# Kernel optimization log

Hardware: AMD Instinct MI355X
Metric: run time of the kernel (lower is better)

The kernel has to match this reference:

```python
import jax, jax.numpy as jnp
import numpy as np


def setup_inputs() -> dict:
    key = jax.random.key(0)
    k1, k2, k3, k4 = jax.random.split(key, 4)
    B, H, S, E, L = 2, 12, 256, 64, 25
    return {
        "attention_probs": jax.random.uniform(k1, (B, H, S, S), dtype=jnp.float32),
        "value_attentions": jax.random.normal(k2, (B, H, S, E), dtype=jnp.float32),
        "relative_positions": jax.random.normal(k3, (B, S, S, H * E), dtype=jnp.float32),
        "W": jax.random.normal(k4, (L, H * E), dtype=jnp.float32) * 0.02,
        "b": jnp.zeros((L,), dtype=jnp.float32),
    }


def reference(attention_probs, value_attentions, relative_positions, W, b):
    # Faithful translation of TransformerMHSLayer.forward:
    #   out[b,h,i,j,e] = p[b,h,i,j] * (v[b,h,j,e] + rel[b,i,j,h,e])
    #   pre[b,j,i,l]   = sum_{h,e} out[b,h,i,j,e] * W[l, h*E+e] + bias[l]
    #   logits[b,j,l,i] = pre[b,j,i,l]
    B, H, S, E = value_attentions.shape
    L = W.shape[0]
    Wr = W.reshape(L, H, E)                       # [L,H,E], matches h*E+e flattening
    rel = relative_positions.reshape(B, S, S, H, E)  # view(B,S,S,H,E)
    # value term: contract v with W per head, then weight by attention probs
    pre = jnp.einsum('bhij,bhje,lhe->bjil', attention_probs, value_attentions, Wr)
    # relative-position term (same attention weighting)
    pre = pre + jnp.einsum('bhij,bijhe,lhe->bjil', attention_probs, rel, Wr)
    pre = pre + b                                  # bias over label dim
    return pre.transpose(0, 1, 3, 2)               # [B, S(j), L, S(i)]
```

## Files before the change

kernel.cpp:

```cpp
#include <hip/hip_runtime.h>
#include <stdint.h>


#define Bb 2
#define Hh 12
#define Ss 256
#define Ee 64
#define Ll 25
#define Kk 768

typedef __attribute__((ext_vector_type(8))) short bf16x8;
typedef __attribute__((ext_vector_type(4))) float f32x4;

#define NFRAG (Hh * 4)
#define AB_BYTES ((size_t)NFRAG * 64 * 8 * 2)
#define PT_BYTES ((size_t)Bb * Ss * Hh * Ss * 4)
#define WV_BYTES ((size_t)Bb * Ss * Hh * 32 * 4)

__device__ __forceinline__ ushort f2bf(float x) {
    union { float f; uint32_t u; } u; u.f = x;
    uint32_t r = u.u + 0x7fff + ((u.u >> 16) & 1);
    return (ushort)(r >> 16);
}

__global__ void a_pack_kernel(const float* __restrict__ W, ushort* __restrict__ ab) {
    int idx = blockIdx.x * 256 + threadIdx.x;
    if (idx >= NFRAG * 64) return;
    int lane = idx & 63, fi = idx >> 6;
    int Lt = fi & 1, ks = (fi >> 1) & 1, h = fi >> 2;
    int l = Lt * 16 + (lane & 15);
    int k0 = h * Ee + ks * 32 + (lane >> 4) * 8;
    ushort* dst = ab + (size_t)idx * 8;
#pragma unroll
    for (int t = 0; t < 8; ++t)
        dst[t] = (l < Ll) ? f2bf(W[l * Kk + k0 + t]) : (ushort)0;
}

__global__ void p_transpose_kernel(const float* __restrict__ p,
                                   float* __restrict__ pt) {
    __shared__ float tile[32][33];
    const int bh = blockIdx.y;
    const int b = bh / Hh, h = bh % Hh;
    const int ti = blockIdx.x >> 3, tj = blockIdx.x & 7;
    const int tx = threadIdx.x & 31, ty = threadIdx.x >> 5;
#pragma unroll
    for (int s = 0; s < 4; ++s) {
        const int il = ty + 8 * s;
        tile[il][tx] = p[((size_t)(b * Hh + h) * Ss + ti * 32 + il) * Ss + tj * 32 + tx];
    }
    __syncthreads();
#pragma unroll
    for (int s = 0; s < 4; ++s) {
        const int jl = ty + 8 * s;
        pt[((size_t)(b * Ss + tj * 32 + jl) * Hh + h) * Ss + ti * 32 + tx] = tile[tx][jl];
    }
}

__global__ void wv_kernel(const float* __restrict__ W, const float* __restrict__ v,
                          float* __restrict__ wv) {
    const int bj = blockIdx.x;
    const int b = bj >> 8, j = bj & (Ss - 1);
    const int t = threadIdx.x;
    const int h = t >> 5, l = t & 31;
    float acc = 0.f;
    if (l < Ll) {
        const float* wrow = W + l * Kk + h * Ee;
        const float* vrow = v + ((size_t)(b * Hh + h) * Ss + j) * Ee;
#pragma unroll
        for (int e = 0; e < Ee; ++e) acc = __builtin_fmaf(wrow[e], vrow[e], acc);
    }
    wv[((size_t)bj * Hh + h) * 32 + l] = acc;
}

struct Ops {
    float4 c0, c1, c2, c3;
    bf16x8 A00, A01, A10, A11;
    float4 w0, w1;
    float pv;
};

__global__ __launch_bounds__(256, 4) void mhs_pipe(
    const float* __restrict__ pt,
    const float* __restrict__ rel,
    const ushort* __restrict__ ab,
    const float* __restrict__ wv,
    const float* __restrict__ bias,
    float* __restrict__ out)
{
    const int g = blockIdx.x;
    const int ig = g & 3, j = (g >> 2) & (Ss - 1), b = g >> 10;
    const int tid = threadIdx.x;
    const int w = tid >> 6, lane = tid & 63;
    const int col = lane & 15, grp = lane >> 4;
    const int iw = ig * 64 + w * 16 + col;

    const float* relp = rel + ((size_t)(b * Ss + iw) * Ss + j) * Kk + grp * 8;
    const ushort* abl = ab + lane * 8;
    const float* wvb = wv + ((size_t)(b * Ss + j) * Hh) * 32 + grp * 4;
    const float* ptb = pt + ((size_t)(b * Ss + j) * Hh) * Ss + iw;

    f32x4 acc0 = {0.f, 0.f, 0.f, 0.f};
    f32x4 acc1 = {0.f, 0.f, 0.f, 0.f};

    auto load_ops = [&](Ops& o, int h) {
        const float* rb = relp + h * Ee;
        o.c0 = *(const float4*)(rb);
        o.c1 = *(const float4*)(rb + 4);
        o.c2 = *(const float4*)(rb + 32);
        o.c3 = *(const float4*)(rb + 36);
        const ushort* ap = abl + (size_t)h * 2048;
        o.A00 = *(const bf16x8*)(ap);
        o.A01 = *(const bf16x8*)(ap + 512);
        o.A10 = *(const bf16x8*)(ap + 1024);
        o.A11 = *(const bf16x8*)(ap + 1536);
        const float* wp = wvb + h * 32;
        o.w0 = *(const float4*)(wp);
        o.w1 = *(const float4*)(wp + 16);
        o.pv = ptb[h * Ss];
    };

    auto compute = [&](const Ops& o) {
        bf16x8 B0, B1;
#pragma unroll
        for (int t = 0; t < 4; ++t) {
            B0[t]     = (short)f2bf(((const float*)&o.c0)[t]);
            B0[t + 4] = (short)f2bf(((const float*)&o.c1)[t]);
            B1[t]     = (short)f2bf(((const float*)&o.c2)[t]);
            B1[t + 4] = (short)f2bf(((const float*)&o.c3)[t]);
        }
        f32x4 C0 = {0.f, 0.f, 0.f, 0.f}, C1 = {0.f, 0.f, 0.f, 0.f};
        C0 = __builtin_amdgcn_mfma_f32_16x16x32_bf16(o.A00, B0, C0, 0, 0, 0);
        C0 = __builtin_amdgcn_mfma_f32_16x16x32_bf16(o.A10, B1, C0, 0, 0, 0);
        C1 = __builtin_amdgcn_mfma_f32_16x16x32_bf16(o.A01, B0, C1, 0, 0, 0);
        C1 = __builtin_amdgcn_mfma_f32_16x16x32_bf16(o.A11, B1, C1, 0, 0, 0);
        const f32x4 wv0 = {o.w0.x, o.w0.y, o.w0.z, o.w0.w};
        const f32x4 wv1 = {o.w1.x, o.w1.y, o.w1.z, o.w1.w};
        acc0 += o.pv * (C0 + wv0);
        acc1 += o.pv * (C1 + wv1);
    };

    Ops oa, ob;
    load_ops(oa, 0);
#pragma unroll 1
    for (int h = 0; h < Hh; h += 2) {
        load_ops(ob, h + 1);
        compute(oa);
        load_ops(oa, (h + 2 < Hh) ? h + 2 : Hh - 1);
        compute(ob);
    }

#pragma unroll
    for (int r = 0; r < 4; ++r) {
        const int l0 = grp * 4 + r;
        out[((size_t)(b * Ss + j) * Ll + l0) * Ss + iw] = acc0[r] + bias[l0];
        const int l1 = 16 + grp * 4 + r;
        if (l1 < Ll)
            out[((size_t)(b * Ss + j) * Ll + l1) * Ss + iw] = acc1[r] + bias[l1];
    }
}

__global__ __launch_bounds__(256, 4) void mhs_basic(
    const float* __restrict__ p, const float* __restrict__ v,
    const float* __restrict__ rel, const float* __restrict__ W,
    const float* __restrict__ bias, float* __restrict__ out)
{
    const int g = blockIdx.x;
    const int ig = g & 3, j = (g >> 2) & (Ss - 1), b = g >> 10;
    const int tid = threadIdx.x;
    const int w = tid >> 6, lane = tid & 63;
    const int col = lane & 15, grp = lane >> 4;
    const int iw = ig * 64 + w * 16 + col;
    const float* relp = rel + ((size_t)(b * Ss + iw) * Ss + j) * Kk + grp * 8;

    f32x4 acc0 = {0.f, 0.f, 0.f, 0.f}, acc1 = {0.f, 0.f, 0.f, 0.f};
#pragma unroll 1
    for (int h = 0; h < Hh; ++h) {
        bf16x8 A00, A01, A10, A11;
#pragma unroll
        for (int t = 0; t < 8; ++t) {
            const int kb = h * Ee + grp * 8 + t;
            const int la = col, lb = 16 + col;
            A00[t] = (short)f2bf(W[la * Kk + kb]);
            A01[t] = (lb < Ll) ? (short)f2bf(W[lb * Kk + kb]) : (short)0;
            A10[t] = (short)f2bf(W[la * Kk + kb + 32]);
            A11[t] = (lb < Ll) ? (short)f2bf(W[lb * Kk + kb + 32]) : (short)0;
        }
        const float* vbp = v + ((size_t)(b * Hh + h) * Ss + j) * Ee + grp * 8;
        const float4 va0 = *(const float4*)(vbp);
        const float4 va1 = *(const float4*)(vbp + 4);
        const float4 vc0 = *(const float4*)(vbp + 32);
        const float4 vc1 = *(const float4*)(vbp + 36);
        const float* rb = relp + h * Ee;
        const float4 c0 = *(const float4*)(rb);
        const float4 c1 = *(const float4*)(rb + 4);
        const float4 c2 = *(const float4*)(rb + 32);
        const float4 c3 = *(const float4*)(rb + 36);
        const float pv = p[((size_t)(b * Hh + h) * Ss + iw) * Ss + j];
        bf16x8 B0, B1;
#pragma unroll
        for (int t = 0; t < 4; ++t) {
            B0[t]     = (short)f2bf(((const float*)&c0)[t] + ((const float*)&va0)[t]);
            B0[t + 4] = (short)f2bf(((const float*)&c1)[t] + ((const float*)&va1)[t]);
            B1[t]     = (short)f2bf(((const float*)&c2)[t] + ((const float*)&vc0)[t]);
            B1[t + 4] = (short)f2bf(((const float*)&c3)[t] + ((const float*)&vc1)[t]);
        }
        f32x4 C0 = {0.f, 0.f, 0.f, 0.f}, C1 = {0.f, 0.f, 0.f, 0.f};
        C0 = __builtin_amdgcn_mfma_f32_16x16x32_bf16(A00, B0, C0, 0, 0, 0);
        C0 = __builtin_amdgcn_mfma_f32_16x16x32_bf16(A10, B1, C0, 0, 0, 0);
        C1 = __builtin_amdgcn_mfma_f32_16x16x32_bf16(A01, B0, C1, 0, 0, 0);
        C1 = __builtin_amdgcn_mfma_f32_16x16x32_bf16(A11, B1, C1, 0, 0, 0);
        acc0 += pv * C0;
        acc1 += pv * C1;
    }
#pragma unroll
    for (int r = 0; r < 4; ++r) {
        const int l0 = grp * 4 + r;
        out[((size_t)(b * Ss + j) * Ll + l0) * Ss + iw] = acc0[r] + bias[l0];
        const int l1 = 16 + grp * 4 + r;
        if (l1 < Ll)
            out[((size_t)(b * Ss + j) * Ll + l1) * Ss + iw] = acc1[r] + bias[l1];
    }
}

extern "C" void kernel_launch(void* const* d_in, const int* in_sizes, int n_in,
                              void* d_out, int out_size, void* d_ws, size_t ws_size,
                              hipStream_t stream) {
    const float* p    = (const float*)d_in[0];
    const float* v    = (const float*)d_in[1];
    const float* rel  = (const float*)d_in[2];
    const float* W    = (const float*)d_in[3];
    const float* bias = (const float*)d_in[4];
    float* out = (float*)d_out;

    const int nblk = Bb * Ss * 4;
    const bool full = ws_size >= AB_BYTES + PT_BYTES + WV_BYTES;

    if (full) {
        ushort* ab = (ushort*)d_ws;
        float* pt = (float*)((char*)d_ws + AB_BYTES);
        float* wvp = (float*)((char*)d_ws + AB_BYTES + PT_BYTES);
        hipLaunchKernelGGL(a_pack_kernel, dim3((NFRAG * 64 + 255) / 256), dim3(256),
                           0, stream, W, ab);
        hipLaunchKernelGGL(p_transpose_kernel, dim3(64, Bb * Hh), dim3(256),
                           0, stream, p, pt);
        hipLaunchKernelGGL(wv_kernel, dim3(Bb * Ss), dim3(Hh * 32),
                           0, stream, W, v, wvp);
        hipLaunchKernelGGL(mhs_pipe, dim3(nblk), dim3(256), 0, stream,
                           pt, rel, ab, wvp, bias, out);
    } else {
        hipLaunchKernelGGL(mhs_basic, dim3(nblk), dim3(256), 0, stream,
                           p, v, rel, W, bias, out);
    }
}
```

Baseline: 124.5 us.

## Fold attention prob into B operand, accumulate in MFMA, swizzle block order

Scales the rel values by the attention prob before bf16 conversion so the MFMAs accumulate straight into acc0/acc1. This removes the per-head zeroed temporaries and the vector multiply-add after each head. The value term (p·wv) moves out of the pipelined loop into a separate post-loop reduction, which shrinks the per-head register buffer. Block indices are also remapped in an interleaved order to change which j/b tiles run concurrently, likely for cache or memory-channel locality. Rounding the p-scaled product to bf16 changes numerics slightly, and the post-loop reads p and wv a second time.

```diff
diff --git a/kernel.cpp b/kernel.cpp
--- a/kernel.cpp
+++ b/kernel.cpp
@@ -72,14 +72,13 @@
     wv[((size_t)bj * Hh + h) * 32 + l] = acc;
 }
 
-struct Ops {
-    float4 c0, c1, c2, c3;
+struct Buf {
+    float4 r0, r1, r2, r3;
     bf16x8 A00, A01, A10, A11;
-    float4 w0, w1;
     float pv;
 };
 
-__global__ __launch_bounds__(256, 4) void mhs_pipe(
+__global__ __launch_bounds__(256, 4) void mhs_pipe2(
     const float* __restrict__ pt,
     const float* __restrict__ rel,
     const ushort* __restrict__ ab,
@@ -87,8 +86,8 @@
     const float* __restrict__ bias,
     float* __restrict__ out)
 {
-    const int g = blockIdx.x;
-    const int ig = g & 3, j = (g >> 2) & (Ss - 1), b = g >> 10;
+    const int m = (blockIdx.x & 7) * 256 + (blockIdx.x >> 3);
+    const int ig = m & 3, j = (m >> 2) & (Ss - 1), b = m >> 10;
     const int tid = threadIdx.x;
     const int w = tid >> 6, lane = tid & 63;
     const int col = lane & 15, grp = lane >> 4;
@@ -96,58 +95,64 @@
 
     const float* relp = rel + ((size_t)(b * Ss + iw) * Ss + j) * Kk + grp * 8;
     const ushort* abl = ab + lane * 8;
+    const float* ptb = pt + ((size_t)(b * Ss + j) * Hh) * Ss + iw;
     const float* wvb = wv + ((size_t)(b * Ss + j) * Hh) * 32 + grp * 4;
-    const float* ptb = pt + ((size_t)(b * Ss + j) * Hh) * Ss + iw;
 
     f32x4 acc0 = {0.f, 0.f, 0.f, 0.f};
     f32x4 acc1 = {0.f, 0.f, 0.f, 0.f};
 
-    auto load_ops = [&](Ops& o, int h) {
+    auto load = [&](Buf& o, int h) {
         const float* rb = relp + h * Ee;
-        o.c0 = *(const float4*)(rb);
-        o.c1 = *(const float4*)(rb + 4);
-        o.c2 = *(const float4*)(rb + 32);
-        o.c3 = *(const float4*)(rb + 36);
+        o.r0 = *(const float4*)(rb);
+        o.r1 = *(const float4*)(rb + 4);
+        o.r2 = *(const float4*)(rb + 32);
+        o.r3 = *(const float4*)(rb + 36);
         const ushort* ap = abl + (size_t)h * 2048;
         o.A00 = *(const bf16x8*)(ap);
         o.A01 = *(const bf16x8*)(ap + 512);
         o.A10 = *(const bf16x8*)(ap + 1024);
         o.A11 = *(const bf16x8*)(ap + 1536);
-        const float* wp = wvb + h * 32;
-        o.w0 = *(const float4*)(wp);
-        o.w1 = *(const float4*)(wp + 16);
         o.pv = ptb[h * Ss];
     };
 
-    auto compute = [&](const Ops& o) {
+    auto compute = [&](const Buf& o) {
+        const float s = o.pv;
         bf16x8 B0, B1;
 #pragma unroll
         for (int t = 0; t < 4; ++t) {
-            B0[t]     = (short)f2bf(((const float*)&o.c0)[t]);
-            B0[t + 4] = (short)f2bf(((const float*)&o.c1)[t]);
-            B1[t]     = (short)f2bf(((const float*)&o.c2)[t]);
-            B1[t + 4] = (short)f2bf(((const float*)&o.c3)[t]);
+            B0[t]     = (short)f2bf(s * ((const float*)&o.r0)[t]);
+            B0[t + 4] = (short)f2bf(s * ((const float*)&o.r1)[t]);
+            B1[t]     = (short)f2bf(s * ((const float*)&o.r2)[t]);
+            B1[t + 4] = (short)f2bf(s * ((const float*)&o.r3)[t]);
         }
-        f32x4 C0 = {0.f, 0.f, 0.f, 0.f}, C1 = {0.f, 0.f, 0.f, 0.f};
-        C0 = __builtin_amdgcn_mfma_f32_16x16x32_bf16(o.A00, B0, C0, 0, 0, 0);
-        C0 = __builtin_amdgcn_mfma_f32_16x16x32_bf16(o.A10, B1, C0, 0, 0, 0);
-        C1 = __builtin_amdgcn_mfma_f32_16x16x32_bf16(o.A01, B0, C1, 0, 0, 0);
-        C1 = __builtin_amdgcn_mfma_f32_16x16x32_bf16(o.A11, B1, C1, 0, 0, 0);
-        const f32x4 wv0 = {o.w0.x, o.w0.y, o.w0.z, o.w0.w};
-        const f32x4 wv1 = {o.w1.x, o.w1.y, o.w1.z, o.w1.w};
-        acc0 += o.pv * (C0 + wv0);
-        acc1 += o.pv * (C1 + wv1);
+        acc0 = __builtin_amdgcn_mfma_f32_16x16x32_bf16(o.A00, B0, acc0, 0, 0, 0);
+        acc0 = __builtin_amdgcn_mfma_f32_16x16x32_bf16(o.A10, B1, acc0, 0, 0, 0);
+        acc1 = __builtin_amdgcn_mfma_f32_16x16x32_bf16(o.A01, B0, acc1, 0, 0, 0);
+        acc1 = __builtin_amdgcn_mfma_f32_16x16x32_bf16(o.A11, B1, acc1, 0, 0, 0);
     };
 
-    Ops oa, ob;
-    load_ops(oa, 0);
+    Buf oa, ob;
+    load(oa, 0);
 #pragma unroll 1
     for (int h = 0; h < Hh; h += 2) {
-        load_ops(ob, h + 1);
+        load(ob, h + 1);
         compute(oa);
-        load_ops(oa, (h + 2 < Hh) ? h + 2 : Hh - 1);
+        if (h + 2 < Hh) load(oa, h + 2);
         compute(ob);
     }
+
+    f32x4 val0 = {0.f, 0.f, 0.f, 0.f};
+    f32x4 val1 = {0.f, 0.f, 0.f, 0.f};
+#pragma unroll
+    for (int h = 0; h < Hh; ++h) {
+        const float pvh = ptb[h * Ss];
+        const f32x4 w0 = *(const f32x4*)(wvb + h * 32);
+        const f32x4 w1 = *(const f32x4*)(wvb + h * 32 + 16);
+        val0 += pvh * w0;
+        val1 += pvh * w1;
+    }
+    acc0 += val0;
+    acc1 += val1;
 
 #pragma unroll
     for (int r = 0; r < 4; ++r) {
@@ -245,7 +250,7 @@
                            0, stream, p, pt);
         hipLaunchKernelGGL(wv_kernel, dim3(Bb * Ss), dim3(Hh * 32),
                            0, stream, W, v, wvp);
-        hipLaunchKernelGGL(mhs_pipe, dim3(nblk), dim3(256), 0, stream,
+        hipLaunchKernelGGL(mhs_pipe2, dim3(nblk), dim3(256), 0, stream,
                            pt, rel, ab, wvp, bias, out);
     } else {
         hipLaunchKernelGGL(mhs_basic, dim3(nblk), dim3(256), 0, stream,
```

After: 123.6 us. About the same (-0.8%).
